# Kernel optimization log

Hardware: AMD Instinct MI355X
Metric: run time of the kernel (lower is better)

The kernel has to match this reference:

```python
import jax, jax.numpy as jnp
import numpy as np

S = 16          # state_dim
H = 96          # hidden_dim
A = 64          # num_actions
B = 256         # batch_size
D_IN = S * S * 64      # 16384
D_H = H * H            # 9216
SPLIT = D_H - S * S    # 8960, action/selection split point


def setup_inputs() -> dict:
    key = jax.random.key(0)
    ks = jax.random.split(key, 14)
    s = jax.random.normal(ks[0], (B, S, S, 64), dtype=jnp.float32)
    mask = jax.random.randint(ks[1], (B, S, S), 0, 2).astype(bool)
    u = jax.random.uniform(ks[2], (B, S * S), dtype=jnp.float32,
                           minval=1e-6, maxval=1.0 - 1e-6)
    def lin(k, fin, fout):
        kw, kb = jax.random.split(k)
        sc = 1.0 / np.sqrt(fin)
        return (jax.random.uniform(kw, (fin, fout), minval=-sc, maxval=sc, dtype=jnp.float32),
                jax.random.uniform(kb, (fout,), minval=-sc, maxval=sc, dtype=jnp.float32))
    W1, b1 = lin(ks[3], D_IN, D_H)
    W2, b2 = lin(ks[4], D_H, D_H)
    W3, b3 = lin(ks[5], D_H, D_H)
    Wa, ba = lin(ks[6], SPLIT, A)
    Ws, bs = lin(ks[7], S * S, S * S)
    return {"s": s, "mask": mask, "u": u, "W1": W1, "b1": b1, "W2": W2,
            "b2": b2, "W3": W3, "b3": b3, "Wa": Wa, "ba": ba, "Ws": Ws, "bs": bs}


def reference(s, mask, u, W1, b1, W2, b2, W3, b3, Wa, ba, Ws, bs):
    x = s.reshape(s.shape[0], -1).astype(jnp.float32)        # [B, D_IN]
    x = jax.nn.relu(x @ W1 + b1)                             # [B, D_H]
    x = jax.nn.relu(x @ W2 + b2)
    x = jax.nn.relu(x @ W3 + b3)
    x_action = jax.nn.softmax(x[:, :SPLIT] @ Wa + ba, axis=1)  # [B, A]
    # selection branch
    p = jax.nn.softmax(x[:, SPLIT:] @ Ws + bs, axis=1)         # [B, S*S]
    m = mask.reshape(mask.shape[0], -1)                        # [B, S*S]
    p = jnp.where(m, -1e9, p)        # masked_fill on the probs (faithful)
    p = jax.nn.softmax(p, axis=1)
    # parallel Gumbel-max == Categorical over valid (unnormalized) probs
    gumbel = -jnp.log(-jnp.log(u))
    scores = jnp.where(m, -jnp.inf, jnp.log(p) + gumbel)
    idx = jnp.argmax(scores, axis=1)                           # [B]
    coordinate = jnp.stack([idx // S, idx % S], axis=1)        # [B, 2]
    sel_prob = jnp.take_along_axis(p, idx[:, None], axis=1)    # [B, 1]
    final_action_prob = x_action * sel_prob                    # [B, A]
    return final_action_prob, coordinate
```

## Files before the change

kernel.cpp:

```cpp
#include <hip/hip_runtime.h>
#include <hip/hip_fp16.h>


typedef _Float16 f16;
typedef _Float16 f16x4 __attribute__((ext_vector_type(4)));
typedef _Float16 f16x8 __attribute__((ext_vector_type(8)));
typedef float f32x4 __attribute__((ext_vector_type(4)));

#define DH 9216
#define SPLIT 8960

__device__ __forceinline__ void gload16(const void* g, void* l) {
    __builtin_amdgcn_global_load_lds(
        (const __attribute__((address_space(1))) void*)g,
        (__attribute__((address_space(3))) void*)l, 16, 0, 0);
}

__global__ void cvt_kernel(const float* __restrict__ in, f16* __restrict__ out, int n) {
    for (int i = (blockIdx.x * blockDim.x + threadIdx.x) * 4; i < n;
         i += gridDim.x * blockDim.x * 4) {
        float4 v = *(const float4*)(in + i);
        f16x4 h = {(_Float16)v.x, (_Float16)v.y, (_Float16)v.z, (_Float16)v.w};
        *(f16x4*)(out + i) = h;
    }
}

__global__ __launch_bounds__(256, 3) void gemm_kernel(
    const f16* __restrict__ A, int K, int Kh, int yshift,
    const float* __restrict__ W,
    float* __restrict__ P)
{
    __shared__ __align__(16) char lds[2][24576];
    const int bid  = blockIdx.x;
    const int y    = bid & ((1 << yshift) - 1);
    const int rem  = bid >> yshift;
    const int m0   = (rem & 1) << 7;
    const int n0   = (rem >> 1) << 7;
    const int tid  = threadIdx.x;
    const int lane = tid & 63;
    const int wid  = tid >> 6;
    const int wm   = wid >> 1, wn = wid & 1;
    const int kbase = y * Kh;
    const int ns   = Kh >> 5;

    f32x4 acc[4][4] = {};

    const float* wsrc0;
    const float* wsrc1;
    const float* wsrc2;
    const float* wsrc3;
    {
        int g0 = tid,      k0 = g0 >> 5, c0 = (g0 & 31) ^ ((5 * (k0 >> 3)) & 31);
        int g1 = tid + 256, k1 = g1 >> 5, c1 = (g1 & 31) ^ ((5 * (k1 >> 3)) & 31);
        int g2 = tid + 512, k2 = g2 >> 5, c2 = (g2 & 31) ^ ((5 * (k2 >> 3)) & 31);
        int g3 = tid + 768, k3 = g3 >> 5, c3 = (g3 & 31) ^ ((5 * (k3 >> 3)) & 31);
        wsrc0 = W + (size_t)(kbase + k0) * DH + n0 + (c0 << 2);
        wsrc1 = W + (size_t)(kbase + k1) * DH + n0 + (c1 << 2);
        wsrc2 = W + (size_t)(kbase + k2) * DH + n0 + (c2 << 2);
        wsrc3 = W + (size_t)(kbase + k3) * DH + n0 + (c3 << 2);
    }
    const f16* asrc0;
    const f16* asrc1;
    {
        int h0 = tid, h1 = tid + 256;
        int r0 = m0 + ((h0 >> 8) << 6) + (((h0 >> 6) & 3) << 4) + (h0 & 15);
        int r1 = m0 + ((h1 >> 8) << 6) + (((h1 >> 6) & 3) << 4) + (h1 & 15);
        asrc0 = A + (size_t)r0 * K + kbase + (((h0 >> 4) & 3) << 3);
        asrc1 = A + (size_t)r1 * K + kbase + (((h1 >> 4) & 3) << 3);
    }

    auto issue = [&](int slot) {
        char* dst = &lds[slot][0];
        gload16(wsrc0, dst + (size_t)tid * 16);          wsrc0 += 32 * DH;
        gload16(wsrc1, dst + (size_t)(tid + 256) * 16);  wsrc1 += 32 * DH;
        gload16(wsrc2, dst + (size_t)(tid + 512) * 16);  wsrc2 += 32 * DH;
        gload16(wsrc3, dst + (size_t)(tid + 768) * 16);  wsrc3 += 32 * DH;
        gload16(asrc0, dst + 16384 + (size_t)tid * 16);         asrc0 += 32;
        gload16(asrc1, dst + 16384 + (size_t)(tid + 256) * 16); asrc1 += 32;
    };

    const int q  = lane >> 4;
    const int lc = lane & 15;
    auto step = [&](int slot) {
        const float* wl = (const float*)&lds[slot][0];
        const f16*   al = (const f16*)&lds[slot][16384];
        f16x8 af[4], bf[4];
#pragma unroll
        for (int ri = 0; ri < 4; ++ri)
            af[ri] = *(const f16x8*)(al + (((wm << 8) + (ri << 6) + lane) << 3));
        const int wbase = (q << 10) + (lc & 3);
#pragma unroll
        for (int ni = 0; ni < 4; ++ni) {
            int p = ((wn << 4) + (ni << 2) + (lc >> 2)) ^ (5 * q);
            int fi = wbase + (p << 2);
            f16x8 b;
#pragma unroll
            for (int j = 0; j < 8; ++j)
                b[j] = (_Float16)wl[fi + (j << 7)];
            bf[ni] = b;
        }
#pragma unroll
        for (int ri = 0; ri < 4; ++ri)
#pragma unroll
            for (int ni = 0; ni < 4; ++ni)
                acc[ri][ni] = __builtin_amdgcn_mfma_f32_16x16x32_f16(
                    af[ri], bf[ni], acc[ri][ni], 0, 0, 0);
    };

    issue(0);
    issue(1);
    __builtin_amdgcn_sched_barrier(0);

    for (int t = 0; t < ns; ++t) {
        if (t + 1 < ns) asm volatile("s_waitcnt vmcnt(6)" ::: "memory");
        else            asm volatile("s_waitcnt vmcnt(0)" ::: "memory");
        __builtin_amdgcn_sched_barrier(0);
        __builtin_amdgcn_s_barrier();
        __builtin_amdgcn_sched_barrier(0);
        step(t & 1);
        __builtin_amdgcn_sched_barrier(0);
        asm volatile("s_waitcnt lgkmcnt(0)" ::: "memory");
        __builtin_amdgcn_sched_barrier(0);
        __builtin_amdgcn_s_barrier();
        __builtin_amdgcn_sched_barrier(0);
        if (t + 2 < ns) {
            issue(t & 1);
            __builtin_amdgcn_sched_barrier(0);
        }
    }

    float* Pb = P + (size_t)y * (256 * DH);
#pragma unroll
    for (int ri = 0; ri < 4; ++ri) {
        int row = m0 + wm * 64 + ri * 16 + (q << 2);
#pragma unroll
        for (int ni = 0; ni < 4; ++ni) {
            int col = n0 + wn * 64 + ni * 16 + lc;
#pragma unroll
            for (int rg = 0; rg < 4; ++rg)
                Pb[(size_t)(row + rg) * DH + col] = acc[ri][ni][rg];
        }
    }
}

__global__ void reduce_kernel(const float* __restrict__ P, int S,
                              const float* __restrict__ bias,
                              f16* __restrict__ oh, float* __restrict__ out32) {
    const int n = 256 * DH;
    for (int i = (blockIdx.x * blockDim.x + threadIdx.x) * 4; i < n;
         i += gridDim.x * blockDim.x * 4) {
        float4 bb = *(const float4*)(bias + (i % DH));
        float4 r = bb;
        for (int j = 0; j < S; ++j) {
            float4 a = *(const float4*)(P + (size_t)j * n + i);
            r.x += a.x; r.y += a.y; r.z += a.z; r.w += a.w;
        }
        r.x = fmaxf(r.x, 0.f); r.y = fmaxf(r.y, 0.f);
        r.z = fmaxf(r.z, 0.f); r.w = fmaxf(r.w, 0.f);
        if (oh) {
            f16x4 h = {(_Float16)r.x, (_Float16)r.y, (_Float16)r.z, (_Float16)r.w};
            *(f16x4*)(oh + i) = h;
        }
        if (out32) *(float4*)(out32 + i) = r;
    }
}

__global__ __launch_bounds__(256) void action_kernel(
    const float* __restrict__ X3, const float* __restrict__ Wa,
    const float* __restrict__ ba, float* __restrict__ xact) {
    __shared__ float xs[SPLIT];
    __shared__ float red[256];
    const int row = blockIdx.x, t = threadIdx.x;
    const float* xr = X3 + (size_t)row * DH;
    for (int k = t * 4; k < SPLIT; k += 1024)
        *(float4*)&xs[k] = *(const float4*)(xr + k);
    __syncthreads();
    const int col = t & 63, kqq = t >> 6;
    float acc = 0.f;
    for (int k = kqq * 2240; k < (kqq + 1) * 2240; ++k)
        acc += xs[k] * Wa[(size_t)k * 64 + col];
    red[t] = acc;
    __syncthreads();
    if (t < 64) {
        float z = red[t] + red[t + 64] + red[t + 128] + red[t + 192] + ba[t];
        float mx = z;
        for (int off = 32; off; off >>= 1) mx = fmaxf(mx, __shfl_xor(mx, off));
        float e = expf(z - mx);
        float s = e;
        for (int off = 32; off; off >>= 1) s += __shfl_xor(s, off);
        xact[row * 64 + t] = e / s;
    }
}

__global__ __launch_bounds__(256) void select_kernel(
    const float* __restrict__ X3, const float* __restrict__ Ws,
    const float* __restrict__ bs, const void* __restrict__ maskp,
    const float* __restrict__ u, const float* __restrict__ xact,
    float* __restrict__ out) {
    __shared__ float xs[256];
    __shared__ float psh[256];
    __shared__ float rr[4];
    __shared__ float bestv[4];
    __shared__ int besti[4];
    __shared__ int sIdx;
    __shared__ int smode;
    const int row = blockIdx.x, t = threadIdx.x;
    const int lane = t & 63, wid = t >> 6;

    if (t < 64) {
        unsigned v = ((const unsigned*)maskp)[t];
        int okInt  = __all(v <= 1u);
        int okByte = __all((v & 0xFEFEFEFEu) == 0u);
        if (t == 0) smode = okInt ? 0 : (okByte ? 1 : 2);
    }
    xs[t] = X3[(size_t)row * DH + SPLIT + t];
    __syncthreads();

    bool mk;
    if (smode == 0)       mk = ((const int*)maskp)[row * 256 + t] != 0;
    else if (smode == 1)  mk = ((const unsigned char*)maskp)[row * 256 + t] != 0;
    else                  mk = ((const float*)maskp)[row * 256 + t] != 0.0f;

    float z = bs[t];
    for (int k = 0; k < 256; ++k)
        z += xs[k] * Ws[k * 256 + t];

    float v = z;
    for (int off = 32; off; off >>= 1) v = fmaxf(v, __shfl_xor(v, off));
    if (lane == 0) rr[wid] = v;
    __syncthreads();
    float m1 = fmaxf(fmaxf(rr[0], rr[1]), fmaxf(rr[2], rr[3]));
    __syncthreads();
    float e1 = expf(z - m1);
    v = e1;
    for (int off = 32; off; off >>= 1) v += __shfl_xor(v, off);
    if (lane == 0) rr[wid] = v;
    __syncthreads();
    float s1 = rr[0] + rr[1] + rr[2] + rr[3];
    __syncthreads();
    float p1 = e1 / s1;

    float q = mk ? -1e9f : p1;
    v = q;
    for (int off = 32; off; off >>= 1) v = fmaxf(v, __shfl_xor(v, off));
    if (lane == 0) rr[wid] = v;
    __syncthreads();
    float m2 = fmaxf(fmaxf(rr[0], rr[1]), fmaxf(rr[2], rr[3]));
    __syncthreads();
    float e2 = expf(q - m2);
    v = e2;
    for (int off = 32; off; off >>= 1) v += __shfl_xor(v, off);
    if (lane == 0) rr[wid] = v;
    __syncthreads();
    float s2 = rr[0] + rr[1] + rr[2] + rr[3];
    float p2 = e2 / s2;
    psh[t] = p2;

    float g = -logf(-logf(u[row * 256 + t]));
    float sc = mk ? -INFINITY : (logf(p2) + g);
    float bv = sc;
    int bi = t;
    for (int off = 32; off; off >>= 1) {
        float ov = __shfl_xor(bv, off);
        int oi = __shfl_xor(bi, off);
        if (ov > bv || (ov == bv && oi < bi)) { bv = ov; bi = oi; }
    }
    if (lane == 0) { bestv[wid] = bv; besti[wid] = bi; }
    __syncthreads();
    if (t == 0) {
        float fv = bestv[0];
        int fi = besti[0];
        for (int w = 1; w < 4; ++w)
            if (bestv[w] > fv || (bestv[w] == fv && besti[w] < fi)) {
                fv = bestv[w]; fi = besti[w];
            }
        sIdx = fi;
    }
    __syncthreads();
    const int idx = sIdx;
    const float sp = psh[idx];
    if (t < 64) out[row * 64 + t] = xact[row * 64 + t] * sp;
    if (t == 0) {
        out[256 * 64 + row * 2 + 0] = (float)(idx >> 4);
        out[256 * 64 + row * 2 + 1] = (float)(idx & 15);
    }
}

extern "C" void kernel_launch(void* const* d_in, const int* in_sizes, int n_in,
                              void* d_out, int out_size, void* d_ws, size_t ws_size,
                              hipStream_t stream) {
    const float* s  = (const float*)d_in[0];
    const void*  mask = d_in[1];
    const float* u  = (const float*)d_in[2];
    const float* W1 = (const float*)d_in[3];
    const float* b1 = (const float*)d_in[4];
    const float* W2 = (const float*)d_in[5];
    const float* b2 = (const float*)d_in[6];
    const float* W3 = (const float*)d_in[7];
    const float* b3 = (const float*)d_in[8];
    const float* Wa = (const float*)d_in[9];
    const float* ba = (const float*)d_in[10];
    const float* Ws = (const float*)d_in[11];
    const float* bs = (const float*)d_in[12];
    float* out = (float*)d_out;
    char* ws = (char*)d_ws;

    f16*   A0 = (f16*)(ws + 0);
    f16*   X1 = (f16*)(ws + 8388608);
    f16*   X2 = (f16*)(ws + 0);
    float* X3 = (float*)(ws + 13107200);
    float* XA = (float*)(ws + 22544384);
    float* P  = (float*)(ws + 22609920);

    const size_t pbytes = 9437184ull;
    int yshift = (ws_size >= 22609920ull + 8 * pbytes) ? 3 : 2;
    const int S = 1 << yshift;

    cvt_kernel<<<2048, 256, 0, stream>>>(s, A0, 256 * 16384);

    const int nblk = (2 * 72) << yshift;
    gemm_kernel<<<nblk, 256, 0, stream>>>(A0, 16384, 16384 / S, yshift, W1, P);
    reduce_kernel<<<1152, 256, 0, stream>>>(P, S, b1, X1, nullptr);
    gemm_kernel<<<nblk, 256, 0, stream>>>(X1, DH, DH / S, yshift, W2, P);
    reduce_kernel<<<1152, 256, 0, stream>>>(P, S, b2, X2, nullptr);
    gemm_kernel<<<nblk, 256, 0, stream>>>(X2, DH, DH / S, yshift, W3, P);
    reduce_kernel<<<1152, 256, 0, stream>>>(P, S, b3, nullptr, X3);

    action_kernel<<<256, 256, 0, stream>>>(X3, Wa, ba, XA);
    select_kernel<<<256, 256, 0, stream>>>(X3, Ws, bs, mask, u, XA, out);
}
```

Baseline: 592.1 us.

## Cover full batch per block with 512 threads, load A directly to registers

The GEMM block now covers all 256 batch rows for a 128-column slice using 8 waves, so each W tile is fetched once instead of twice across the two M-halves. The A operand is loaded straight from global memory into registers with double buffering (even/odd), which removes the A staging through LDS and shrinks LDS per block. The loop is unrolled by two to alternate buffers. Tradeoffs: half as many blocks, higher register pressure from the A buffers, and possibly less coalesced global A loads.

```diff
diff --git a/kernel.cpp b/kernel.cpp
--- a/kernel.cpp
+++ b/kernel.cpp
@@ -25,17 +25,15 @@
     }
 }
 
-__global__ __launch_bounds__(256, 3) void gemm_kernel(
+__global__ __launch_bounds__(512, 2) void gemm_kernel(
     const f16* __restrict__ A, int K, int Kh, int yshift,
     const float* __restrict__ W,
     float* __restrict__ P)
 {
-    __shared__ __align__(16) char lds[2][24576];
+    __shared__ __align__(16) char lds[2][16384];
     const int bid  = blockIdx.x;
     const int y    = bid & ((1 << yshift) - 1);
-    const int rem  = bid >> yshift;
-    const int m0   = (rem & 1) << 7;
-    const int n0   = (rem >> 1) << 7;
+    const int n0   = (bid >> yshift) << 7;
     const int tid  = threadIdx.x;
     const int lane = tid & 63;
     const int wid  = tid >> 6;
@@ -44,55 +42,39 @@
     const int ns   = Kh >> 5;
 
     f32x4 acc[4][4] = {};
+    f16x8 aE[4], aO[4];
 
     const float* wsrc0;
     const float* wsrc1;
-    const float* wsrc2;
-    const float* wsrc3;
     {
-        int g0 = tid,      k0 = g0 >> 5, c0 = (g0 & 31) ^ ((5 * (k0 >> 3)) & 31);
-        int g1 = tid + 256, k1 = g1 >> 5, c1 = (g1 & 31) ^ ((5 * (k1 >> 3)) & 31);
-        int g2 = tid + 512, k2 = g2 >> 5, c2 = (g2 & 31) ^ ((5 * (k2 >> 3)) & 31);
-        int g3 = tid + 768, k3 = g3 >> 5, c3 = (g3 & 31) ^ ((5 * (k3 >> 3)) & 31);
+        int g0 = tid,       k0 = g0 >> 5, c0 = (g0 & 31) ^ ((5 * (k0 >> 3)) & 31);
+        int g1 = tid + 512, k1 = g1 >> 5, c1 = (g1 & 31) ^ ((5 * (k1 >> 3)) & 31);
         wsrc0 = W + (size_t)(kbase + k0) * DH + n0 + (c0 << 2);
         wsrc1 = W + (size_t)(kbase + k1) * DH + n0 + (c1 << 2);
-        wsrc2 = W + (size_t)(kbase + k2) * DH + n0 + (c2 << 2);
-        wsrc3 = W + (size_t)(kbase + k3) * DH + n0 + (c3 << 2);
-    }
-    const f16* asrc0;
-    const f16* asrc1;
-    {
-        int h0 = tid, h1 = tid + 256;
-        int r0 = m0 + ((h0 >> 8) << 6) + (((h0 >> 6) & 3) << 4) + (h0 & 15);
-        int r1 = m0 + ((h1 >> 8) << 6) + (((h1 >> 6) & 3) << 4) + (h1 & 15);
-        asrc0 = A + (size_t)r0 * K + kbase + (((h0 >> 4) & 3) << 3);
-        asrc1 = A + (size_t)r1 * K + kbase + (((h1 >> 4) & 3) << 3);
-    }
-
-    auto issue = [&](int slot) {
-        char* dst = &lds[slot][0];
-        gload16(wsrc0, dst + (size_t)tid * 16);          wsrc0 += 32 * DH;
-        gload16(wsrc1, dst + (size_t)(tid + 256) * 16);  wsrc1 += 32 * DH;
-        gload16(wsrc2, dst + (size_t)(tid + 512) * 16);  wsrc2 += 32 * DH;
-        gload16(wsrc3, dst + (size_t)(tid + 768) * 16);  wsrc3 += 32 * DH;
-        gload16(asrc0, dst + 16384 + (size_t)tid * 16);         asrc0 += 32;
-        gload16(asrc1, dst + 16384 + (size_t)(tid + 256) * 16); asrc1 += 32;
-    };
-
+    }
     const int q  = lane >> 4;
     const int lc = lane & 15;
-    auto step = [&](int slot) {
+    const f16* abase = A + (size_t)(wm * 64 + lc) * K + kbase + (q << 3);
+
+    auto issueW = [&](int slot) {
+        char* dst = &lds[slot][0];
+        gload16(wsrc0, dst + (size_t)tid * 16);         wsrc0 += 32 * DH;
+        gload16(wsrc1, dst + (size_t)(tid + 512) * 16); wsrc1 += 32 * DH;
+    };
+    auto loadA = [&](f16x8* a, int t) {
+        const f16* p = abase + (t << 5);
+#pragma unroll
+        for (int ri = 0; ri < 4; ++ri)
+            a[ri] = *(const f16x8*)(p + (size_t)(ri << 4) * K);
+    };
+    auto mfma_step = [&](int slot, f16x8* a) {
         const float* wl = (const float*)&lds[slot][0];
-        const f16*   al = (const f16*)&lds[slot][16384];
-        f16x8 af[4], bf[4];
-#pragma unroll
-        for (int ri = 0; ri < 4; ++ri)
-            af[ri] = *(const f16x8*)(al + (((wm << 8) + (ri << 6) + lane) << 3));
         const int wbase = (q << 10) + (lc & 3);
+        f16x8 bf[4];
 #pragma unroll
         for (int ni = 0; ni < 4; ++ni) {
             int p = ((wn << 4) + (ni << 2) + (lc >> 2)) ^ (5 * q);
-            int fi = wbase + (p << 2);
+            int fi = wbase + ((p & 31) << 2);
             f16x8 b;
 #pragma unroll
             for (int j = 0; j < 8; ++j)
@@ -104,27 +86,41 @@
 #pragma unroll
             for (int ni = 0; ni < 4; ++ni)
                 acc[ri][ni] = __builtin_amdgcn_mfma_f32_16x16x32_f16(
-                    af[ri], bf[ni], acc[ri][ni], 0, 0, 0);
+                    a[ri], bf[ni], acc[ri][ni], 0, 0, 0);
     };
 
-    issue(0);
-    issue(1);
+    issueW(0); loadA(aE, 0);
+    issueW(1); loadA(aO, 1);
     __builtin_amdgcn_sched_barrier(0);
 
-    for (int t = 0; t < ns; ++t) {
-        if (t + 1 < ns) asm volatile("s_waitcnt vmcnt(6)" ::: "memory");
+    for (int t = 0; t < ns; t += 2) {
+        asm volatile("s_waitcnt vmcnt(6)" ::: "memory");
+        __builtin_amdgcn_sched_barrier(0);
+        __builtin_amdgcn_s_barrier();
+        __builtin_amdgcn_sched_barrier(0);
+        mfma_step(0, aE);
+        __builtin_amdgcn_sched_barrier(0);
+        asm volatile("s_waitcnt lgkmcnt(0)" ::: "memory");
+        __builtin_amdgcn_sched_barrier(0);
+        __builtin_amdgcn_s_barrier();
+        __builtin_amdgcn_sched_barrier(0);
+        if (t + 2 < ns) {
+            issueW(0); loadA(aE, t + 2);
+            __builtin_amdgcn_sched_barrier(0);
+        }
+        if (t + 2 < ns) asm volatile("s_waitcnt vmcnt(6)" ::: "memory");
         else            asm volatile("s_waitcnt vmcnt(0)" ::: "memory");
         __builtin_amdgcn_sched_barrier(0);
         __builtin_amdgcn_s_barrier();
         __builtin_amdgcn_sched_barrier(0);
-        step(t & 1);
+        mfma_step(1, aO);
         __builtin_amdgcn_sched_barrier(0);
         asm volatile("s_waitcnt lgkmcnt(0)" ::: "memory");
         __builtin_amdgcn_sched_barrier(0);
         __builtin_amdgcn_s_barrier();
         __builtin_amdgcn_sched_barrier(0);
-        if (t + 2 < ns) {
-            issue(t & 1);
+        if (t + 3 < ns) {
+            issueW(1); loadA(aO, t + 3);
             __builtin_amdgcn_sched_barrier(0);
         }
     }
@@ -132,7 +128,7 @@
     float* Pb = P + (size_t)y * (256 * DH);
 #pragma unroll
     for (int ri = 0; ri < 4; ++ri) {
-        int row = m0 + wm * 64 + ri * 16 + (q << 2);
+        int row = wm * 64 + ri * 16 + (q << 2);
 #pragma unroll
         for (int ni = 0; ni < 4; ++ni) {
             int col = n0 + wn * 64 + ni * 16 + lc;
@@ -318,12 +314,12 @@
 
     cvt_kernel<<<2048, 256, 0, stream>>>(s, A0, 256 * 16384);
 
-    const int nblk = (2 * 72) << yshift;
-    gemm_kernel<<<nblk, 256, 0, stream>>>(A0, 16384, 16384 / S, yshift, W1, P);
+    const int nblk = 72 << yshift;
+    gemm_kernel<<<nblk, 512, 0, stream>>>(A0, 16384, 16384 / S, yshift, W1, P);
     reduce_kernel<<<1152, 256, 0, stream>>>(P, S, b1, X1, nullptr);
-    gemm_kernel<<<nblk, 256, 0, stream>>>(X1, DH, DH / S, yshift, W2, P);
+    gemm_kernel<<<nblk, 512, 0, stream>>>(X1, DH, DH / S, yshift, W2, P);
     reduce_kernel<<<1152, 256, 0, stream>>>(P, S, b2, X2, nullptr);
-    gemm_kernel<<<nblk, 256, 0, stream>>>(X2, DH, DH / S, yshift, W3, P);
+    gemm_kernel<<<nblk, 512, 0, stream>>>(X2, DH, DH / S, yshift, W3, P);
     reduce_kernel<<<1152, 256, 0, stream>>>(P, S, b3, nullptr, X3);
 
     action_kernel<<<256, 256, 0, stream>>>(X3, Wa, ba, XA);
```

Result: slower. 783.4 us (+32.3%).
